# Kernel optimization log

Hardware: AMD Instinct MI355X
Metric: run time of the kernel (lower is better)

## Reference

```python
import jax, jax.numpy as jnp
import numpy as np
import math

H = 4096; NH = 32; QLR = 1536; KVLR = 512
DN = 128; DR = 64; DV = 128; QD = DN + DR  # q_head_dim = 192
B = 1; S = 2048
BASE = 50000.0; FACTOR = 32.0; ORIG_MAX = 4096; BETA_FAST = 32.0; BETA_SLOW = 1.0
EPS = 1e-6
_M = 0.1 * 1.0 * math.log(FACTOR) + 1.0  # yarn mscale (mscale_all_dim=1)
SCALE = (QD ** -0.5) * _M * _M


def _yarn_cos_sin(seq_len):
    dim = DR
    f = np.arange(0, dim, 2, dtype=np.float32) / dim
    freq_extra = 1.0 / BASE ** f
    freq_inter = 1.0 / (FACTOR * BASE ** f)
    def corr(nr):
        return dim * math.log(ORIG_MAX / (nr * 2 * math.pi)) / (2 * math.log(BASE))
    low = max(math.floor(corr(BETA_FAST)), 0)
    high = min(math.ceil(corr(BETA_SLOW)), dim - 1)
    hi = high + 0.001 if low == high else float(high)
    ramp = np.clip((np.arange(dim // 2, dtype=np.float32) - low) / (hi - low), 0.0, 1.0)
    inv_freq_mask = 1.0 - ramp
    inv_freq = freq_inter * (1.0 - inv_freq_mask) + freq_extra * inv_freq_mask
    t = np.arange(seq_len, dtype=np.float32)
    fr = np.outer(t, inv_freq)
    emb = np.concatenate([fr, fr], axis=-1)
    # mscale ratio = get_mscale(f,1)/get_mscale(f,1) = 1.0
    return jnp.asarray(np.cos(emb)), jnp.asarray(np.sin(emb))


def _rms(x, w):
    v = jnp.mean(x.astype(jnp.float32) ** 2, axis=-1, keepdims=True)
    return w * (x.astype(jnp.float32) * jax.lax.rsqrt(v + EPS)).astype(x.dtype)


def _reorder(x):
    # interleaved -> [evens, odds] (matches view(d//2,2).transpose.reshape)
    d = x.shape[-1]
    x = x.reshape(x.shape[:-1] + (d // 2, 2))
    return jnp.concatenate([x[..., 0], x[..., 1]], axis=-1)


def _rotate_half(x):
    h = x.shape[-1] // 2
    return jnp.concatenate([-x[..., h:], x[..., :h]], axis=-1)


def _rope(x, cos, sin):
    x = _reorder(x)
    return x * cos + _rotate_half(x) * sin


def setup_inputs() -> dict:
    key = jax.random.key(0)
    ks = jax.random.split(key, 6)
    hs = jax.random.normal(ks[0], (B, S, H), dtype=jnp.float32)
    causal = jnp.tril(jnp.ones((S, S), dtype=bool))
    mask = jnp.where(causal, 0.0, -1e9).astype(jnp.float32)[None, None]
    pos = jnp.broadcast_to(jnp.arange(S, dtype=jnp.int64 if jax.config.jax_enable_x64 else jnp.int32), (B, S))
    def w(k, shape, fan_in):
        return jax.random.normal(k, shape, dtype=jnp.float32) * (fan_in ** -0.5)
    return {
        "hidden_states": hs,
        "attention_mask": mask,
        "position_ids": pos,
        "q_a_w": w(ks[1], (QLR, H), H),
        "q_a_ln_w": jnp.ones((QLR,), jnp.float32),
        "q_b_w": w(ks[2], (NH * QD, QLR), QLR),
        "kv_a_w": w(ks[3], (KVLR + DR, H), H),
        "kv_a_ln_w": jnp.ones((KVLR,), jnp.float32),
        "kv_b_w": w(ks[4], (NH * (DN + DV), KVLR), KVLR),
        "o_w": w(ks[5], (H, NH * DV), NH * DV),
    }


def reference(hidden_states, attention_mask, position_ids, q_a_w, q_a_ln_w, q_b_w, kv_a_w, kv_a_ln_w, kv_b_w, o_w):
    b, s, _ = hidden_states.shape
    q = _rms(hidden_states @ q_a_w.T, q_a_ln_w) @ q_b_w.T
    q = q.reshape(b, s, NH, QD).transpose(0, 2, 1, 3)          # [b,h,s,192]
    q_nope, q_pe = q[..., :DN], q[..., DN:]
    ckv = hidden_states @ kv_a_w.T                              # [b,s,576]
    comp, k_pe = ckv[..., :KVLR], ckv[..., KVLR:]
    k_pe = k_pe.reshape(b, s, 1, DR).transpose(0, 2, 1, 3)      # [b,1,s,64]
    kv = (_rms(comp, kv_a_ln_w) @ kv_b_w.T).reshape(b, s, NH, DN + DV).transpose(0, 2, 1, 3)
    k_nope, v = kv[..., :DN], kv[..., DN:]
    cos, sin = _yarn_cos_sin(s)
    cos = cos[position_ids][:, None]                            # [b,1,s,64]
    sin = sin[position_ids][:, None]
    q_pe = _rope(q_pe, cos, sin)
    k_pe = _rope(k_pe, cos, sin)
    qs = jnp.concatenate([q_nope, q_pe], axis=-1)               # [b,h,s,192]
    ks = jnp.concatenate([k_nope, jnp.broadcast_to(k_pe, (b, NH, s, DR))], axis=-1)
    aw = jnp.einsum('bhqd,bhkd->bhqk', qs, ks) * SCALE
    aw = jax.nn.softmax((aw + attention_mask).astype(jnp.float32), axis=-1).astype(hidden_states.dtype)
    out = jnp.einsum('bhqk,bhkd->bhqd', aw, v)                  # [b,h,s,128]
    out = out.transpose(0, 2, 1, 3).reshape(b, s, NH * DV)
    return out @ o_w.T
```

## Files before the change

kernel.cpp:

```cpp
#include <hip/hip_runtime.h>
#include <hip/hip_fp16.h>

typedef _Float16 f16x8 __attribute__((ext_vector_type(8)));
typedef float f32x4 __attribute__((ext_vector_type(4)));
typedef float f32x16 __attribute__((ext_vector_type(16)));

#define DEV __device__ __forceinline__

typedef const __attribute__((address_space(1))) void gvoid_t;
typedef __attribute__((address_space(3))) void lvoid_t;

DEV void gload16(const void* g, void* l) {
  __builtin_amdgcn_global_load_lds((gvoid_t*)g, (lvoid_t*)l, 16, 0, 0);
}

DEV f32x4 mfma16(f16x8 a, f16x8 b, f32x4 c) {
  return __builtin_amdgcn_mfma_f32_16x16x32_f16(a, b, c, 0, 0, 0);
}

DEV f32x16 mfma32(f16x8 a, f16x8 b, f32x16 c) {
  return __builtin_amdgcn_mfma_f32_32x32x16_f16(a, b, c, 0, 0, 0);
}

__global__ __launch_bounds__(256) void cvt_kernel(const float* __restrict__ s,
                                                  __half* __restrict__ d, int n4) {
  int stride = gridDim.x * 256;
  for (int i = blockIdx.x * 256 + threadIdx.x; i < n4; i += stride) {
    float4 v = ((const float4*)s)[i];
    __align__(8) __half a[4] = {__float2half(v.x), __float2half(v.y),
                                __float2half(v.z), __float2half(v.w)};
    *((uint2*)(d + (size_t)i * 4)) = *((uint2*)a);
  }
}

__global__ __launch_bounds__(256) void cvt5_kernel(const float* __restrict__ s0,
                                                   const float* __restrict__ s1,
                                                   const float* __restrict__ s2,
                                                   const float* __restrict__ s3,
                                                   const float* __restrict__ s4,
                                                   __half* __restrict__ d0, __half* __restrict__ d1,
                                                   __half* __restrict__ d2, __half* __restrict__ d3,
                                                   __half* __restrict__ d4) {
  const int c0 = 2097152, c1 = 3670016, c2 = 4259840, c3 = 6619136, c4 = 7667712;
  int stride = gridDim.x * 256;
  for (int i = blockIdx.x * 256 + threadIdx.x; i < c4; i += stride) {
    const float* s;
    __half* d;
    int j;
    if (i < c0) { s = s0; d = d0; j = i; }
    else if (i < c1) { s = s1; d = d1; j = i - c0; }
    else if (i < c2) { s = s2; d = d2; j = i - c1; }
    else if (i < c3) { s = s3; d = d3; j = i - c2; }
    else { s = s4; d = d4; j = i - c3; }
    float4 v = ((const float4*)s)[j];
    __align__(8) __half a[4] = {__float2half(v.x), __float2half(v.y),
                                __float2half(v.z), __float2half(v.w)};
    *((uint2*)(d + (size_t)j * 4)) = *((uint2*)a);
  }
}

__global__ __launch_bounds__(256) void norm_rope_kernel(const float* __restrict__ qab,
                                                        const float* __restrict__ q_ln,
                                                        const float* __restrict__ kv_ln,
                                                        const float2* __restrict__ cs,
                                                        __half* __restrict__ qa_r,
                                                        __half* __restrict__ kv_r,
                                                        __half* __restrict__ Kb) {
  const int row = blockIdx.x, tid = threadIdx.x;
  const float* xr = qab + (size_t)row * 2112;
  float4 a0 = ((const float4*)xr)[tid];
  float4 a1 = make_float4(0.f, 0.f, 0.f, 0.f);
  float4 b0 = make_float4(0.f, 0.f, 0.f, 0.f);
  if (tid < 128) {
    a1 = ((const float4*)xr)[256 + tid];
    b0 = ((const float4*)(xr + 1536))[tid];
  }
  float sq = a0.x * a0.x + a0.y * a0.y + a0.z * a0.z + a0.w * a0.w +
             a1.x * a1.x + a1.y * a1.y + a1.z * a1.z + a1.w * a1.w;
  float sk = b0.x * b0.x + b0.y * b0.y + b0.z * b0.z + b0.w * b0.w;
  for (int mm = 1; mm <= 32; mm <<= 1) {
    sq += __shfl_xor(sq, mm);
    sk += __shfl_xor(sk, mm);
  }
  __shared__ float r1[4], r2[4];
  __shared__ __half ro[64];
  if ((tid & 63) == 0) { r1[tid >> 6] = sq; r2[tid >> 6] = sk; }
  if (tid < 32) {
    float x0 = xr[2048 + 2 * tid], x1 = xr[2048 + 2 * tid + 1];
    float2 c = cs[row * 32 + tid];
    ro[tid] = __float2half(x0 * c.x - x1 * c.y);
    ro[32 + tid] = __float2half(x1 * c.x + x0 * c.y);
  }
  __syncthreads();
  float rsq = rsqrtf((r1[0] + r1[1] + r1[2] + r1[3]) * (1.f / 1536.f) + 1e-6f);
  float rsk = rsqrtf((r2[0] + r2[1] + r2[2] + r2[3]) * (1.f / 512.f) + 1e-6f);
  __half* yq = qa_r + (size_t)row * 1536;
  {
    int j = tid * 4;
    yq[j + 0] = __float2half(q_ln[j + 0] * a0.x * rsq);
    yq[j + 1] = __float2half(q_ln[j + 1] * a0.y * rsq);
    yq[j + 2] = __float2half(q_ln[j + 2] * a0.z * rsq);
    yq[j + 3] = __float2half(q_ln[j + 3] * a0.w * rsq);
  }
  if (tid < 128) {
    int j = 1024 + tid * 4;
    yq[j + 0] = __float2half(q_ln[j + 0] * a1.x * rsq);
    yq[j + 1] = __float2half(q_ln[j + 1] * a1.y * rsq);
    yq[j + 2] = __float2half(q_ln[j + 2] * a1.z * rsq);
    yq[j + 3] = __float2half(q_ln[j + 3] * a1.w * rsq);
    __half* yk = kv_r + (size_t)row * 512;
    int jk = tid * 4;
    yk[jk + 0] = __float2half(kv_ln[jk + 0] * b0.x * rsk);
    yk[jk + 1] = __float2half(kv_ln[jk + 1] * b0.y * rsk);
    yk[jk + 2] = __float2half(kv_ln[jk + 2] * b0.z * rsk);
    yk[jk + 3] = __float2half(kv_ln[jk + 3] * b0.w * rsk);
  }
#pragma unroll
  for (int it = 0; it < 8; ++it) {
    int i = it * 256 + tid;
    int hh = i >> 6, d = i & 63;
    Kb[((size_t)hh * 2048 + row) * 192 + 128 + d] = ro[d];
  }
}

__global__ __launch_bounds__(256) void rope_table_kernel(const int* __restrict__ pos,
                                                         float2* __restrict__ cs) {
  int i = blockIdx.x * 256 + threadIdx.x;
  int row = i >> 5, j = i & 31;
  double f = (double)j * (1.0 / 32.0);
  double fe = exp(-f * 10.81977828441028);
  double fi = fe * (1.0 / 32.0);
  double ramp = fmin(fmax(((double)j - 8.0) * (1.0 / 12.0), 0.0), 1.0);
  double inv = fi * ramp + fe * (1.0 - ramp);
  double ang = (double)pos[row] * inv;
  cs[i] = make_float2((float)cos(ang), (float)sin(ang));
}

__global__ __launch_bounds__(256) void rope_q_kernel(const __half* __restrict__ qpe,
                                                     const float2* __restrict__ cs,
                                                     __half* __restrict__ Qb, float qscale) {
  int i = blockIdx.x * 256 + threadIdx.x;
  int row = i >> 10, rem = i & 1023, h = rem >> 5, j = rem & 31;
  float x0 = __half2float(qpe[(size_t)row * 2048 + h * 64 + 2 * j]);
  float x1 = __half2float(qpe[(size_t)row * 2048 + h * 64 + 2 * j + 1]);
  float2 c = cs[row * 32 + j];
  float o0 = (x0 * c.x - x1 * c.y) * qscale;
  float o1 = (x1 * c.x + x0 * c.y) * qscale;
  __half* dst = Qb + ((size_t)h * 2048 + row) * 192;
  dst[128 + j] = __float2half(o0);
  dst[160 + j] = __float2half(o1);
}

template <int BN, int EPI>
__global__ __launch_bounds__(256) void gemm128(const __half* __restrict__ A, int lda,
                                               const __half* __restrict__ B, int K, int Ncols,
                                               float* __restrict__ Cf, int ldc,
                                               __half* __restrict__ O1, __half* __restrict__ O2,
                                               float qscale) {
  constexpr int NFR = BN / 32;
  __shared__ __align__(16) char As[2 * 128 * 128];
  __shared__ __align__(16) char Bs[2 * BN * 128];
  const int tid = threadIdx.x;
  const int lane = tid & 63, w = tid >> 6;
  const int l15 = lane & 15, g = lane >> 4;
  const int wr = w >> 1, wc = w & 1;
  const int nwg = gridDim.x * gridDim.y;
  int wg = blockIdx.y * gridDim.x + blockIdx.x;
  wg = (wg & 7) * (nwg >> 3) + (wg >> 3);
  const int m0 = (wg / gridDim.x) * 128, n0 = (wg % gridDim.x) * BN;
  const int srow = lane >> 3;
  const int scol = ((lane & 7) ^ srow) * 8;
  f32x4 acc[4][NFR] = {};
  const int nt = K >> 6;

  auto stage = [&](int t, int buf) {
    const __half* Ab = A + t * 64 + scol;
    const __half* Bb = B + t * 64 + scol;
#pragma unroll
    for (int cc = 0; cc < 4; ++cc) {
      int ch = w * 4 + cc;
      gload16(Ab + (size_t)(m0 + ch * 8 + srow) * lda, As + buf * 16384 + ch * 1024);
    }
#pragma unroll
    for (int cc = 0; cc < NFR; ++cc) {
      int ch = w * NFR + cc;
      gload16(Bb + (size_t)(n0 + ch * 8 + srow) * K, Bs + buf * (BN * 128) + ch * 1024);
    }
  };

  stage(0, 0);
  __syncthreads();

  for (int t = 0; t < nt; ++t) {
    const int buf = t & 1;
    if (t + 1 < nt) stage(t + 1, buf ^ 1);
    const char* Ab = As + buf * 16384;
    const char* Bb = Bs + buf * (BN * 128);
#pragma unroll
    for (int kk = 0; kk < 2; ++kk) {
      f16x8 af[4], bf[NFR];
#pragma unroll
      for (int m = 0; m < 4; ++m) {
        int r = wr * 64 + m * 16 + l15;
        af[m] = *(const f16x8*)(Ab + r * 128 + (((kk << 2) | g) ^ (r & 7)) * 16);
      }
#pragma unroll
      for (int n = 0; n < NFR; ++n) {
        int r = wc * (BN / 2) + n * 16 + l15;
        bf[n] = *(const f16x8*)(Bb + r * 128 + (((kk << 2) | g) ^ (r & 7)) * 16);
      }
#pragma unroll
      for (int m = 0; m < 4; ++m)
#pragma unroll
        for (int n = 0; n < NFR; ++n) acc[m][n] = mfma16(af[m], bf[n], acc[m][n]);
    }
    __syncthreads();
  }

#pragma unroll
  for (int m = 0; m < 4; ++m)
#pragma unroll
    for (int n = 0; n < NFR; ++n)
#pragma unroll
      for (int i = 0; i < 4; ++i) {
        int row = m0 + wr * 64 + m * 16 + g * 4 + i;
        int col = n0 + wc * (BN / 2) + n * 16 + l15;
        float v = acc[m][n][i];
        if (EPI == 0) {
          if (col < Ncols) Cf[(size_t)row * ldc + col] = v;
        } else if (EPI == 2) {
          int h = col / 192, d = col - h * 192;
          if (d < 128)
            O1[((size_t)h * 2048 + row) * 192 + d] = __float2half(v * qscale);
          else
            O2[(size_t)row * 2048 + h * 64 + (d - 128)] = __float2half(v);
        } else if (EPI == 3) {
          int h = col >> 8, d = col & 255;
          if (d < 128)
            O1[((size_t)h * 2048 + row) * 192 + d] = __float2half(v);
          else
            O2[((size_t)h * 128 + (d - 128)) * 2048 + row] = __float2half(v);
        }
      }
}

__global__ __launch_bounds__(256, 2) void attn_kernel(const __half* __restrict__ Q,
                                                      const __half* __restrict__ K,
                                                      const __half* __restrict__ Vt,
                                                      __half* __restrict__ Out) {
  __shared__ __align__(16) char Klds[2 * 64 * 384];
  __shared__ __align__(16) char Vlds[2 * 128 * 128];
  int wg = blockIdx.y * gridDim.x + blockIdx.x;
  wg = (wg & 7) * 64 + (wg >> 3);
  const int h = wg >> 4, qt = 15 - (wg & 15);
  const int q0 = qt * 128;
  const int nt = 2 * qt + 2;
  const int tid = threadIdx.x, lane = tid & 63, w = tid >> 6;
  const int l31 = lane & 31, hf = lane >> 5;
  const int qrow = q0 + w * 32 + l31;
  const int maskT = (w < 2) ? nt - 2 : nt - 1;

  const char* Kg = (const char*)(K + (size_t)h * 2048 * 192);
  const char* Vg = (const char*)(Vt + (size_t)h * 128 * 2048);

  int kRow[6], kSS[6];
#pragma unroll
  for (int cc = 0; cc < 6; ++cc) {
    int c = w * 6 + cc;
    int L = c * 64 + lane;
    int row = (L * 2731) >> 16;
    int slot = L - row * 24;
    kRow[cc] = row;
    kSS[cc] = (slot & ~7) | ((slot ^ row) & 7);
  }
  int vD[4], vSS[4];
#pragma unroll
  for (int cc = 0; cc < 4; ++cc) {
    int c = w * 4 + cc;
    int L = c * 64 + lane;
    int d = L >> 3, slot = L & 7;
    vD[cc] = d;
    vSS[cc] = slot ^ (d & 7);
  }

  const __half* Qh = Q + ((size_t)h * 2048 + qrow) * 192;
  f16x8 qf[12];
#pragma unroll
  for (int dblk = 0; dblk < 12; ++dblk)
    qf[dblk] = *(const f16x8*)(Qh + dblk * 16 + hf * 8);

  f32x16 acc[4] = {};
  float m_i = -1e30f, l_i = 0.f;

#pragma unroll
  for (int cc = 0; cc < 6; ++cc)
    gload16(Kg + (size_t)kRow[cc] * 384 + kSS[cc] * 16, Klds + (w * 6 + cc) * 1024);
#pragma unroll
  for (int cc = 0; cc < 4; ++cc)
    gload16(Vg + ((size_t)vD[cc] * 2048) * 2 + vSS[cc] * 16, Vlds + (w * 4 + cc) * 1024);
  __syncthreads();

  for (int t = 0; t < nt; ++t) {
    const int kv0 = t * 64;
    if (t + 1 < nt) {
      char* Kn = Klds + ((t + 1) & 1) * 24576;
      char* Vn = Vlds + ((t + 1) & 1) * 16384;
#pragma unroll
      for (int cc = 0; cc < 6; ++cc)
        gload16(Kg + (size_t)(kv0 + 64 + kRow[cc]) * 384 + kSS[cc] * 16,
                Kn + (w * 6 + cc) * 1024);
#pragma unroll
      for (int cc = 0; cc < 4; ++cc)
        gload16(Vg + ((size_t)vD[cc] * 2048 + kv0 + 64) * 2 + vSS[cc] * 16,
                Vn + (w * 4 + cc) * 1024);
    }

    if (t <= maskT) {
      const char* Kc = Klds + (t & 1) * 24576;
      const char* Vc = Vlds + (t & 1) * 16384;
      f32x16 sT0 = {}, sT1 = {};
#pragma unroll
      for (int dblk = 0; dblk < 12; ++dblk) {
        int row0 = l31, slot = dblk * 2 + hf;
        int ss0 = (slot & ~7) | ((slot ^ row0) & 7);
        f16x8 kf0 = *(const f16x8*)(Kc + row0 * 384 + ss0 * 16);
        sT0 = mfma32(kf0, qf[dblk], sT0);
        int row1 = 32 + l31;
        int ss1 = (slot & ~7) | ((slot ^ row1) & 7);
        f16x8 kf1 = *(const f16x8*)(Kc + row1 * 384 + ss1 * 16);
        sT1 = mfma32(kf1, qf[dblk], sT1);
      }
      float ps[32];
#pragma unroll
      for (int r = 0; r < 16; ++r) { ps[r] = sT0[r]; ps[16 + r] = sT1[r]; }
      if (t == maskT) {
#pragma unroll
        for (int kb = 0; kb < 2; ++kb)
#pragma unroll
          for (int r = 0; r < 16; ++r) {
            int kg = kv0 + kb * 32 + (r & 3) + 8 * (r >> 2) + 4 * hf;
            if (kg > qrow) ps[kb * 16 + r] = -1e30f;
          }
      }
      float mt = ps[0];
#pragma unroll
      for (int r = 1; r < 32; ++r) mt = fmaxf(mt, ps[r]);
      mt = fmaxf(mt, __shfl_xor(mt, 32));
      float nm = fmaxf(m_i, mt);
      if (__any(mt - m_i > 8.f)) {
        float corr = exp2f(m_i - nm);
        m_i = nm;
        l_i *= corr;
#pragma unroll
        for (int nb = 0; nb < 4; ++nb)
#pragma unroll
          for (int r = 0; r < 16; ++r) acc[nb][r] *= corr;
      }
      float rs = 0.f;
      unsigned pk[16];
#pragma unroll
      for (int r = 0; r < 16; ++r) {
        float pa = exp2f(ps[2 * r] - m_i);
        float pb = exp2f(ps[2 * r + 1] - m_i);
        rs += pa + pb;
        __half2 hh = __floats2half2_rn(pa, pb);
        pk[r] = *(unsigned*)&hh;
      }
      rs += __shfl_xor(rs, 32);
      l_i += rs;
#pragma unroll
      for (int ks = 0; ks < 4; ++ks) {
        int base = (ks >> 1) * 8 + (ks & 1) * 4;
        unsigned q0u = pk[base + 0], q1u = pk[base + 1];
        unsigned q2u = pk[base + 2], q3u = pk[base + 3];
        unsigned s0 = __shfl_xor(q0u, 32), s1 = __shfl_xor(q1u, 32);
        unsigned s2 = __shfl_xor(q2u, 32), s3 = __shfl_xor(q3u, 32);
        union { f16x8 v; unsigned u[4]; } pb_;
        pb_.u[0] = hf ? s2 : q0u;
        pb_.u[1] = hf ? s3 : q1u;
        pb_.u[2] = hf ? q2u : s0;
        pb_.u[3] = hf ? q3u : s1;
#pragma unroll
        for (int nb = 0; nb < 4; ++nb) {
          int d = nb * 32 + l31;
          int ss = (ks * 2 + hf) ^ (d & 7);
          f16x8 vf = *(const f16x8*)(Vc + d * 128 + ss * 16);
          acc[nb] = mfma32(vf, pb_.v, acc[nb]);
        }
      }
    }
    __syncthreads();
  }

  float inv = 1.0f / l_i;
  __half* Or = Out + (size_t)qrow * 4096 + h * 128;
#pragma unroll
  for (int nb = 0; nb < 4; ++nb)
#pragma unroll
    for (int r2 = 0; r2 < 4; ++r2) {
      __align__(8) __half h4[4];
#pragma unroll
      for (int j = 0; j < 4; ++j) h4[j] = __float2half(acc[nb][r2 * 4 + j] * inv);
      *(uint2*)(Or + nb * 32 + r2 * 8 + hf * 4) = *(uint2*)h4;
    }
}

extern "C" void kernel_launch(void* const* d_in, const int* in_sizes, int n_in,
                              void* d_out, int out_size, void* d_ws, size_t ws_size,
                              hipStream_t stream) {
  (void)in_sizes; (void)n_in; (void)out_size; (void)ws_size;
  const float* hs = (const float*)d_in[0];
  const int* pos = (const int*)d_in[2];
  const float* q_a_w = (const float*)d_in[3];
  const float* q_a_ln = (const float*)d_in[4];
  const float* q_b_w = (const float*)d_in[5];
  const float* kv_a_w = (const float*)d_in[6];
  const float* kv_a_ln = (const float*)d_in[7];
  const float* kv_b_w = (const float*)d_in[8];
  const float* o_w = (const float*)d_in[9];

  char* p = (char*)d_ws;
  auto alloc = [&](size_t sz) { char* r = p; p += (sz + 255) & ~(size_t)255; return r; };
  __half* hs_h = (__half*)alloc((size_t)2048 * 4096 * 2);
  __half* w_qab = (__half*)alloc((size_t)2176 * 4096 * 2);
  __half* w_qb = (__half*)alloc((size_t)6144 * 1536 * 2);
  __half* w_kvb = (__half*)alloc((size_t)8192 * 512 * 2);
  float* qab_f = (float*)alloc((size_t)2048 * 2112 * 4);
  __half* qa_r = (__half*)alloc((size_t)2048 * 1536 * 2);
  __half* kv_r = (__half*)alloc((size_t)2048 * 512 * 2);
  float2* cs_tab = (float2*)alloc((size_t)2048 * 32 * 8);
  __half* Qb = (__half*)alloc((size_t)32 * 2048 * 192 * 2);
  __half* Kb = (__half*)alloc((size_t)32 * 2048 * 192 * 2);
  __half* Vtb = (__half*)alloc((size_t)32 * 128 * 2048 * 2);
  __half* qpe = (__half*)alloc((size_t)2048 * 2048 * 2);
  __half* attn_h = hs_h;
  __half* w_o = Qb;

  constexpr float QSCALE = 0.13086090981960297f * 1.4426950408889634f;

  cvt5_kernel<<<2048, 256, 0, stream>>>(hs, q_a_w, kv_a_w, q_b_w, kv_b_w,
                                        hs_h, w_qab, w_qab + (size_t)1536 * 4096,
                                        w_qb, w_kvb);
  rope_table_kernel<<<(2048 * 32) / 256, 256, 0, stream>>>(pos, cs_tab);

  gemm128<192, 0><<<dim3(11, 16), 256, 0, stream>>>(hs_h, 4096, w_qab, 4096, 2112, qab_f,
                                                    2112, nullptr, nullptr, 1.f);
  norm_rope_kernel<<<2048, 256, 0, stream>>>(qab_f, q_a_ln, kv_a_ln, cs_tab,
                                             qa_r, kv_r, Kb);
  gemm128<128, 2><<<dim3(48, 16), 256, 0, stream>>>(qa_r, 1536, w_qb, 1536, 6144, nullptr,
                                                    0, Qb, qpe, QSCALE);
  rope_q_kernel<<<(2048 * 1024) / 256, 256, 0, stream>>>(qpe, cs_tab, Qb, QSCALE);
  gemm128<128, 3><<<dim3(64, 16), 256, 0, stream>>>(kv_r, 512, w_kvb, 512, 8192, nullptr,
                                                    0, Kb, Vtb, 1.f);
  attn_kernel<<<dim3(16, 32), 256, 0, stream>>>(Qb, Kb, Vtb, attn_h);
  cvt_kernel<<<2048, 256, 0, stream>>>(o_w, w_o, (int)((size_t)4096 * 4096 / 4));
  gemm128<128, 0><<<dim3(32, 16), 256, 0, stream>>>(attn_h, 4096, w_o, 4096, 4096,
                                                    (float*)d_out, 4096, nullptr, nullptr,
                                                    1.f);
}
```

Before: 436.5 us.

## Split attention KV tiles across waves with paired causal q-tiles and merge

Reworks the attention kernel so each workgroup processes two 64-row query tiles (pr and 31-pr) to balance causal work, and splits each 64-key tile between wave pairs, with each wave owning 32 keys, then merges the two partial softmax states through LDS at the end. V is now single-buffered and loaded each iteration, with extra barriers between the score and PV phases. The K/V LDS swizzle also gains an extra XOR term to reduce bank conflicts. This aims at load balance and lower per-wave register use, at the cost of more synchronisation, an LDS merge step, and dropping the occupancy hint from launch bounds.

```diff
diff --git a/kernel.cpp b/kernel.cpp
--- a/kernel.cpp
+++ b/kernel.cpp
@@ -244,21 +244,18 @@
       }
 }
 
-__global__ __launch_bounds__(256, 2) void attn_kernel(const __half* __restrict__ Q,
-                                                      const __half* __restrict__ K,
-                                                      const __half* __restrict__ Vt,
-                                                      __half* __restrict__ Out) {
+__global__ __launch_bounds__(256) void attn_kernel(const __half* __restrict__ Q,
+                                                   const __half* __restrict__ K,
+                                                   const __half* __restrict__ Vt,
+                                                   __half* __restrict__ Out) {
   __shared__ __align__(16) char Klds[2 * 64 * 384];
-  __shared__ __align__(16) char Vlds[2 * 128 * 128];
+  __shared__ __align__(16) char Vlds[128 * 128];
   int wg = blockIdx.y * gridDim.x + blockIdx.x;
   wg = (wg & 7) * 64 + (wg >> 3);
-  const int h = wg >> 4, qt = 15 - (wg & 15);
-  const int q0 = qt * 128;
-  const int nt = 2 * qt + 2;
+  const int h = wg >> 4, pr = wg & 15;
   const int tid = threadIdx.x, lane = tid & 63, w = tid >> 6;
   const int l31 = lane & 31, hf = lane >> 5;
-  const int qrow = q0 + w * 32 + l31;
-  const int maskT = (w < 2) ? nt - 2 : nt - 1;
+  const int qsub = w & 1, b = w >> 1;
 
   const char* Kg = (const char*)(K + (size_t)h * 2048 * 192);
   const char* Vg = (const char*)(Vt + (size_t)h * 128 * 2048);
@@ -271,7 +268,7 @@
     int row = (L * 2731) >> 16;
     int slot = L - row * 24;
     kRow[cc] = row;
-    kSS[cc] = (slot & ~7) | ((slot ^ row) & 7);
+    kSS[cc] = (slot & ~7) | ((slot ^ row ^ (row >> 3)) & 7);
   }
   int vD[4], vSS[4];
 #pragma unroll
@@ -280,129 +277,154 @@
     int L = c * 64 + lane;
     int d = L >> 3, slot = L & 7;
     vD[cc] = d;
-    vSS[cc] = slot ^ (d & 7);
-  }
-
-  const __half* Qh = Q + ((size_t)h * 2048 + qrow) * 192;
-  f16x8 qf[12];
-#pragma unroll
-  for (int dblk = 0; dblk < 12; ++dblk)
-    qf[dblk] = *(const f16x8*)(Qh + dblk * 16 + hf * 8);
-
-  f32x16 acc[4] = {};
-  float m_i = -1e30f, l_i = 0.f;
-
-#pragma unroll
-  for (int cc = 0; cc < 6; ++cc)
-    gload16(Kg + (size_t)kRow[cc] * 384 + kSS[cc] * 16, Klds + (w * 6 + cc) * 1024);
-#pragma unroll
-  for (int cc = 0; cc < 4; ++cc)
-    gload16(Vg + ((size_t)vD[cc] * 2048) * 2 + vSS[cc] * 16, Vlds + (w * 4 + cc) * 1024);
-  __syncthreads();
-
-  for (int t = 0; t < nt; ++t) {
-    const int kv0 = t * 64;
-    if (t + 1 < nt) {
-      char* Kn = Klds + ((t + 1) & 1) * 24576;
-      char* Vn = Vlds + ((t + 1) & 1) * 16384;
-#pragma unroll
-      for (int cc = 0; cc < 6; ++cc)
-        gload16(Kg + (size_t)(kv0 + 64 + kRow[cc]) * 384 + kSS[cc] * 16,
-                Kn + (w * 6 + cc) * 1024);
+    vSS[cc] = slot ^ ((d ^ (d >> 3)) & 7);
+  }
+
+  for (int ht = 0; ht < 2; ++ht) {
+    const int qt = ht ? (31 - pr) : pr;
+    const int q0 = qt * 64;
+    const int nt = qt + 1;
+    const int qrow = q0 + qsub * 32 + l31;
+
+    const __half* Qh = Q + ((size_t)h * 2048 + qrow) * 192;
+    f16x8 qf[12];
+#pragma unroll
+    for (int dblk = 0; dblk < 12; ++dblk)
+      qf[dblk] = *(const f16x8*)(Qh + dblk * 16 + hf * 8);
+
+    f32x16 acc[4] = {};
+    float m_i = -1e30f, l_i = 0.f;
+
+#pragma unroll
+    for (int cc = 0; cc < 6; ++cc)
+      gload16(Kg + (size_t)kRow[cc] * 384 + kSS[cc] * 16, Klds + (w * 6 + cc) * 1024);
+    __syncthreads();
+
+    for (int t = 0; t < nt; ++t) {
+      const int kv0 = t * 64;
 #pragma unroll
       for (int cc = 0; cc < 4; ++cc)
-        gload16(Vg + ((size_t)vD[cc] * 2048 + kv0 + 64) * 2 + vSS[cc] * 16,
-                Vn + (w * 4 + cc) * 1024);
-    }
-
-    if (t <= maskT) {
-      const char* Kc = Klds + (t & 1) * 24576;
-      const char* Vc = Vlds + (t & 1) * 16384;
-      f32x16 sT0 = {}, sT1 = {};
-#pragma unroll
-      for (int dblk = 0; dblk < 12; ++dblk) {
-        int row0 = l31, slot = dblk * 2 + hf;
-        int ss0 = (slot & ~7) | ((slot ^ row0) & 7);
-        f16x8 kf0 = *(const f16x8*)(Kc + row0 * 384 + ss0 * 16);
-        sT0 = mfma32(kf0, qf[dblk], sT0);
-        int row1 = 32 + l31;
-        int ss1 = (slot & ~7) | ((slot ^ row1) & 7);
-        f16x8 kf1 = *(const f16x8*)(Kc + row1 * 384 + ss1 * 16);
-        sT1 = mfma32(kf1, qf[dblk], sT1);
-      }
-      float ps[32];
-#pragma unroll
-      for (int r = 0; r < 16; ++r) { ps[r] = sT0[r]; ps[16 + r] = sT1[r]; }
-      if (t == maskT) {
-#pragma unroll
-        for (int kb = 0; kb < 2; ++kb)
+        gload16(Vg + ((size_t)vD[cc] * 2048 + kv0) * 2 + vSS[cc] * 16,
+                Vlds + (w * 4 + cc) * 1024);
+      if (t + 1 < nt) {
+        char* Kn = Klds + ((t + 1) & 1) * 24576;
+#pragma unroll
+        for (int cc = 0; cc < 6; ++cc)
+          gload16(Kg + (size_t)(kv0 + 64 + kRow[cc]) * 384 + kSS[cc] * 16,
+                  Kn + (w * 6 + cc) * 1024);
+      }
+
+      const bool last = (t == nt - 1);
+      const bool skip = last && (w == 2);
+      float ps[16];
+      unsigned pk[8];
+      bool live = !skip;
+      if (live) {
+        const char* Kc = Klds + (t & 1) * 24576;
+        f32x16 sT = {};
+#pragma unroll
+        for (int dblk = 0; dblk < 12; ++dblk) {
+          int row = b * 32 + l31, slot = dblk * 2 + hf;
+          int ss = (slot & ~7) | ((slot ^ row ^ (row >> 3)) & 7);
+          f16x8 kf = *(const f16x8*)(Kc + row * 384 + ss * 16);
+          sT = mfma32(kf, qf[dblk], sT);
+        }
+#pragma unroll
+        for (int r = 0; r < 16; ++r) ps[r] = sT[r];
+        if (last && (qsub == b)) {
 #pragma unroll
           for (int r = 0; r < 16; ++r) {
-            int kg = kv0 + kb * 32 + (r & 3) + 8 * (r >> 2) + 4 * hf;
-            if (kg > qrow) ps[kb * 16 + r] = -1e30f;
+            int kg = kv0 + b * 32 + (r & 3) + 8 * (r >> 2) + 4 * hf;
+            if (kg > qrow) ps[r] = -1e30f;
           }
-      }
-      float mt = ps[0];
-#pragma unroll
-      for (int r = 1; r < 32; ++r) mt = fmaxf(mt, ps[r]);
-      mt = fmaxf(mt, __shfl_xor(mt, 32));
-      float nm = fmaxf(m_i, mt);
-      if (__any(mt - m_i > 8.f)) {
-        float corr = exp2f(m_i - nm);
-        m_i = nm;
-        l_i *= corr;
-#pragma unroll
-        for (int nb = 0; nb < 4; ++nb)
-#pragma unroll
-          for (int r = 0; r < 16; ++r) acc[nb][r] *= corr;
-      }
-      float rs = 0.f;
-      unsigned pk[16];
-#pragma unroll
-      for (int r = 0; r < 16; ++r) {
-        float pa = exp2f(ps[2 * r] - m_i);
-        float pb = exp2f(ps[2 * r + 1] - m_i);
-        rs += pa + pb;
-        __half2 hh = __floats2half2_rn(pa, pb);
-        pk[r] = *(unsigned*)&hh;
-      }
-      rs += __shfl_xor(rs, 32);
-      l_i += rs;
-#pragma unroll
-      for (int ks = 0; ks < 4; ++ks) {
-        int base = (ks >> 1) * 8 + (ks & 1) * 4;
-        unsigned q0u = pk[base + 0], q1u = pk[base + 1];
-        unsigned q2u = pk[base + 2], q3u = pk[base + 3];
-        unsigned s0 = __shfl_xor(q0u, 32), s1 = __shfl_xor(q1u, 32);
-        unsigned s2 = __shfl_xor(q2u, 32), s3 = __shfl_xor(q3u, 32);
-        union { f16x8 v; unsigned u[4]; } pb_;
-        pb_.u[0] = hf ? s2 : q0u;
-        pb_.u[1] = hf ? s3 : q1u;
-        pb_.u[2] = hf ? q2u : s0;
-        pb_.u[3] = hf ? q3u : s1;
-#pragma unroll
-        for (int nb = 0; nb < 4; ++nb) {
-          int d = nb * 32 + l31;
-          int ss = (ks * 2 + hf) ^ (d & 7);
-          f16x8 vf = *(const f16x8*)(Vc + d * 128 + ss * 16);
-          acc[nb] = mfma32(vf, pb_.v, acc[nb]);
-        }
-      }
+        }
+        float mt = ps[0];
+#pragma unroll
+        for (int r = 1; r < 16; ++r) mt = fmaxf(mt, ps[r]);
+        mt = fmaxf(mt, __shfl_xor(mt, 32));
+        float nm = fmaxf(m_i, mt);
+        if (__any(mt - m_i > 8.f)) {
+          float corr = exp2f(m_i - nm);
+          m_i = nm;
+          l_i *= corr;
+#pragma unroll
+          for (int nb = 0; nb < 4; ++nb)
+#pragma unroll
+            for (int r = 0; r < 16; ++r) acc[nb][r] *= corr;
+        }
+        float rs = 0.f;
+#pragma unroll
+        for (int r = 0; r < 8; ++r) {
+          float pa = exp2f(ps[2 * r] - m_i);
+          float pb = exp2f(ps[2 * r + 1] - m_i);
+          rs += pa + pb;
+          __half2 hh = __floats2half2_rn(pa, pb);
+          pk[r] = *(unsigned*)&hh;
+        }
+        rs += __shfl_xor(rs, 32);
+        l_i += rs;
+      }
+      __syncthreads();
+
+      if (live) {
+#pragma unroll
+        for (int ks = 0; ks < 2; ++ks) {
+          int base = ks * 4;
+          unsigned q0u = pk[base + 0], q1u = pk[base + 1];
+          unsigned q2u = pk[base + 2], q3u = pk[base + 3];
+          unsigned s0 = __shfl_xor(q0u, 32), s1 = __shfl_xor(q1u, 32);
+          unsigned s2 = __shfl_xor(q2u, 32), s3 = __shfl_xor(q3u, 32);
+          union { f16x8 v; unsigned u[4]; } pb_;
+          pb_.u[0] = hf ? s2 : q0u;
+          pb_.u[1] = hf ? s3 : q1u;
+          pb_.u[2] = hf ? q2u : s0;
+          pb_.u[3] = hf ? q3u : s1;
+#pragma unroll
+          for (int nb = 0; nb < 4; ++nb) {
+            int d = nb * 32 + l31;
+            int slot = b * 4 + ks * 2 + hf;
+            int ss = slot ^ ((d ^ (d >> 3)) & 7);
+            f16x8 vf = *(const f16x8*)(Vlds + d * 128 + ss * 16);
+            acc[nb] = mfma32(vf, pb_.v, acc[nb]);
+          }
+        }
+      }
+      __syncthreads();
+    }
+
+    float* mbuf = (float*)Klds;
+    if (b == 1) {
+      float* dst = mbuf + (qsub * 64 + lane) * 66;
+      dst[0] = m_i;
+      dst[1] = l_i;
+#pragma unroll
+      for (int nb = 0; nb < 4; ++nb)
+#pragma unroll
+        for (int r = 0; r < 16; ++r) dst[2 + nb * 16 + r] = acc[nb][r];
     }
     __syncthreads();
-  }
-
-  float inv = 1.0f / l_i;
-  __half* Or = Out + (size_t)qrow * 4096 + h * 128;
-#pragma unroll
-  for (int nb = 0; nb < 4; ++nb)
-#pragma unroll
-    for (int r2 = 0; r2 < 4; ++r2) {
-      __align__(8) __half h4[4];
-#pragma unroll
-      for (int j = 0; j < 4; ++j) h4[j] = __float2half(acc[nb][r2 * 4 + j] * inv);
-      *(uint2*)(Or + nb * 32 + r2 * 8 + hf * 4) = *(uint2*)h4;
-    }
+    if (b == 0) {
+      const float* src = mbuf + (qsub * 64 + lane) * 66;
+      float mb = src[0], lb = src[1];
+      float nm = fmaxf(m_i, mb);
+      float ca = exp2f(m_i - nm), cb = exp2f(mb - nm);
+      float inv = 1.0f / (l_i * ca + lb * cb);
+      __half* Or = Out + (size_t)qrow * 4096 + h * 128;
+#pragma unroll
+      for (int nb = 0; nb < 4; ++nb)
+#pragma unroll
+        for (int r2 = 0; r2 < 4; ++r2) {
+          __align__(8) __half h4[4];
+#pragma unroll
+          for (int j = 0; j < 4; ++j) {
+            float v = acc[nb][r2 * 4 + j] * ca + src[2 + nb * 16 + r2 * 4 + j] * cb;
+            h4[j] = __float2half(v * inv);
+          }
+          *(uint2*)(Or + nb * 32 + r2 * 8 + hf * 4) = *(uint2*)h4;
+        }
+    }
+    __syncthreads();
+  }
 }
 
 extern "C" void kernel_launch(void* const* d_in, const int* in_sizes, int n_in,
```

Result: no change. 440.6 us (+0.9%).
